# Kernel tuning notes

Hardware: AMD Instinct MI355X
Metric: run time of the kernel (lower is better)

Reference implementation:

```python
import jax, jax.numpy as jnp
import numpy as np

B, S, D = 2, 2048, 1024
H, DH = 16, 64
BS = 512            # block_size
MAX_LEN = 2048      # rope base = max_seq_length
NB = S // BS        # number of blocks (no padding: S % BS == 0)


def setup_inputs() -> dict:
    key = jax.random.key(0)
    ks = jax.random.split(key, 5)
    s = 1.0 / np.sqrt(D)
    x = jax.random.normal(ks[0], (B, S, D), jnp.float32)
    Wq = jax.random.normal(ks[1], (D, D), jnp.float32) * s
    Wk = jax.random.normal(ks[2], (D, D), jnp.float32) * s
    Wv = jax.random.normal(ks[3], (D, D), jnp.float32) * s
    Wo = jax.random.normal(ks[4], (D, D), jnp.float32) * s
    z = jnp.zeros((D,), jnp.float32)
    return {"x": x, "Wq": Wq, "bq": z, "Wk": Wk, "bk": z,
            "Wv": Wv, "bv": z, "Wo": Wo, "bo": z}


def _apply_rope(q, k):
    # inv_freq uses max_seq_length as the base (as in the source module)
    inv_freq = 1.0 / MAX_LEN ** (jnp.arange(0, DH, 2, dtype=jnp.float32) / DH)  # [DH/2]
    pos = jnp.arange(S, dtype=jnp.float32)
    freqs = jnp.outer(pos, inv_freq)                 # [S, DH/2]
    cos = jnp.cos(freqs)[None, :, None, :]           # [1,S,1,DH/2]
    sin = jnp.sin(freqs)[None, :, None, :]
    half = DH // 2
    q1, q2 = q[..., :half], q[..., half:]
    k1, k2 = k[..., :half], k[..., half:]
    q_rot = jnp.concatenate([q1 * cos - q2 * sin, q1 * sin + q2 * cos], axis=-1)
    k_rot = jnp.concatenate([k1 * cos - k2 * sin, k1 * sin + k2 * cos], axis=-1)
    return q_rot, k_rot


def _block_attn(qb, q_start, kb, vb, k_start):
    # qb,kb,vb: [B,H,BS,DH]; returns attended [B,H,BS,DH], lse [B,H,BS]
    scale = 1.0 / jnp.sqrt(DH)
    scores = jnp.einsum('bhqd,bhkd->bhqk', qb, kb) * scale
    q_pos = jnp.arange(BS) + q_start
    k_pos = jnp.arange(BS) + k_start
    mask = (q_pos[:, None] >= k_pos[None, :])[None, None]   # [1,1,BS,BS]
    scores = jnp.where(mask, scores, -1e9)
    mx = jnp.max(scores, axis=-1, keepdims=True)
    mx = jnp.where(jnp.isinf(mx), 0.0, mx)
    e = jnp.where(mask, jnp.exp(scores - mx), 0.0)
    se = jnp.sum(e, axis=-1, keepdims=True) + 1e-10
    attended = jnp.einsum('bhqk,bhkd->bhqd', e / se, vb)
    lse = (jnp.log(se) + mx)[..., 0]                        # [B,H,BS]
    return attended, lse


def _forward(x, Wq, bq, Wk, bk, Wv, bv, Wo, bo):
    q = (x @ Wq + bq).reshape(B, S, H, DH)
    k = (x @ Wk + bk).reshape(B, S, H, DH)
    v = (x @ Wv + bv).reshape(B, S, H, DH)
    q, k = _apply_rope(q, k)
    # split into blocks: [NB, B, H, BS, DH]
    def to_blocks(t):
        return t.reshape(B, NB, BS, H, DH).transpose(1, 0, 3, 2, 4)
    qb, kb, vb = to_blocks(q), to_blocks(k), to_blocks(v)
    starts = jnp.arange(NB) * BS
    inner = jax.vmap(_block_attn, in_axes=(None, None, 0, 0, 0))   # over k blocks
    outer = jax.vmap(inner, in_axes=(0, 0, None, None, None))      # over q blocks
    att, lse = outer(qb, starts, kb, vb, starts)
    # att: [NBq,NBk,B,H,BS,DH], lse: [NBq,NBk,B,H,BS]
    mlse = jnp.max(lse, axis=1, keepdims=True)
    w = jnp.exp(lse - mlse)
    w = w / (jnp.sum(w, axis=1, keepdims=True) + 1e-10)
    acc = jnp.sum(att * w[..., None], axis=1)                      # [NBq,B,H,BS,DH]
    out = acc.transpose(1, 0, 3, 2, 4).reshape(B, S, D)
    out = out @ Wo + bo
    return out


def reference(x, Wq, bq, Wk, bk, Wv, bv, Wo, bo):
    out = _forward(x, Wq, bq, Wk, bk, Wv, bv, Wo, bo)
    attention_weights = jnp.ones((B, H, S, S), jnp.float32)  # dummy, as in source
    return out, attention_weights
```

## Files before the change

### kernel.cpp

```cpp
#include <hip/hip_runtime.h>
#include <cstdint>
#include <cstddef>

#define DEVINL __device__ __forceinline__

typedef float   f32x4  __attribute__((ext_vector_type(4)));
typedef float   vf4    __attribute__((ext_vector_type(4)));
typedef __bf16  bf16x8 __attribute__((ext_vector_type(8)));
typedef uint32_t u32;
typedef unsigned short u16;
typedef uint32_t u32x4 __attribute__((ext_vector_type(4)));

constexpr int Bb = 2, Ss = 2048, Dd = 1024, Hh = 16;
constexpr int Mm = Bb * Ss;

DEVINL u16 f2bf(float f) {
  union { float f; u32 u; } a; a.f = f;
  u32 r = a.u + 0x7fffu + ((a.u >> 16) & 1u);
  return (u16)(r >> 16);
}

typedef const __attribute__((address_space(1))) void* gas_t;
typedef __attribute__((address_space(3))) void* las_t;
DEVINL void gld_lds16(const void* g, void* l) {
  __builtin_amdgcn_global_load_lds((gas_t)g, (las_t)l, 16, 0, 0);
}

__global__ void fill_ones(vf4* __restrict__ p, long long n4) {
  size_t i = (size_t)blockIdx.x * blockDim.x + threadIdx.x;
  size_t stride = (size_t)gridDim.x * blockDim.x;
  const vf4 one = {1.f, 1.f, 1.f, 1.f};
  for (; i < (size_t)n4; i += stride)
    __builtin_nontemporal_store(one, p + i);
}

__global__ void rope_table(float* __restrict__ cosT, float* __restrict__ sinT) {
  int idx = blockIdx.x * 256 + threadIdx.x;
  int s = idx >> 5, j = idx & 31;
  float freq = (float)s * exp2f(-11.0f * (float)j / 32.0f);
  cosT[idx] = cosf(freq);
  sinT[idx] = sinf(freq);
}

__global__ void cast_x(const float* __restrict__ x, u16* __restrict__ xb) {
  size_t i = ((size_t)blockIdx.x * 256 + threadIdx.x) * 4;
  vf4 v = *(const vf4*)(x + i);
  union { u16 u[4]; unsigned long long q; } o;
  o.u[0] = f2bf(v.x); o.u[1] = f2bf(v.y); o.u[2] = f2bf(v.z); o.u[3] = f2bf(v.w);
  *(unsigned long long*)(xb + i) = o.q;
}

__global__ void transpose_cast_W(const float* __restrict__ W0, const float* __restrict__ W1,
                                 const float* __restrict__ W2, const float* __restrict__ W3,
                                 u16* __restrict__ Wt) {
  __shared__ u16 tile[64][72];
  const int z = blockIdx.z;
  const float* W = (z == 0) ? W0 : (z == 1) ? W1 : (z == 2) ? W2 : W3;
  u16* Out = Wt + (size_t)z * (Dd * Dd);
  const int k0 = blockIdx.x * 64, n0 = blockIdx.y * 64;
  const int tid = threadIdx.x;
#pragma unroll
  for (int it = 0; it < 4; ++it) {
    int r = it * 16 + (tid >> 4);
    int c = (tid & 15) * 4;
    vf4 v = *(const vf4*)(W + (size_t)(k0 + r) * Dd + n0 + c);
    tile[r][c + 0] = f2bf(v.x); tile[r][c + 1] = f2bf(v.y);
    tile[r][c + 2] = f2bf(v.z); tile[r][c + 3] = f2bf(v.w);
  }
  __syncthreads();
#pragma unroll
  for (int it = 0; it < 2; ++it) {
    int c = it * 256 + tid;
    int n = c >> 3, ck = c & 7;
    union { u16 u[8]; u32x4 q; } o;
#pragma unroll
    for (int j = 0; j < 8; ++j) o.u[j] = tile[ck * 8 + j][n];
    *(u32x4*)(Out + (size_t)(n0 + n) * Dd + k0 + ck * 8) = o.q;
  }
}

template <int BM>
DEVINL void gemm_mainloop(const u16* __restrict__ A, const u16* __restrict__ Bt,
                          int m0, int n0, char* lds, f32x4 (&acc)[BM / 32][4],
                          vf4* __restrict__ onesp, size_t obase) {
  constexpr int MT = BM / 32;
  constexpr int ABYTES = BM * 64;
  const int tid = threadIdx.x, lane = tid & 63;
  const int w = tid >> 6, wr = w >> 1, wc = w & 1;
  const int l15 = lane & 15, l4 = lane >> 4;
  char* Ab = lds;
  char* Bb = lds + 2 * ABYTES;
  auto stageA = [&](int k0, char* dst) {
#pragma unroll
    for (int h2 = 0; h2 < BM / 64; ++h2) {
      int c = h2 * 256 + tid;
      const char* src = (const char*)A + (size_t)(m0 + (c >> 2)) * 2048 + k0 * 2 + (c & 3) * 16;
      gld_lds16(src, dst + c * 16);
    }
  };
  auto stageB = [&](int k0, char* dst) {
#pragma unroll
    for (int h2 = 0; h2 < 2; ++h2) {
      int c = h2 * 256 + tid;
      const char* src = (const char*)Bt + (size_t)(n0 + (c >> 2)) * 2048 + k0 * 2 + (c & 3) * 16;
      gld_lds16(src, dst + c * 16);
    }
  };
  stageA(0, Ab);
  stageB(0, Bb);
  __syncthreads();
  const vf4 onev = {1.f, 1.f, 1.f, 1.f};
#pragma unroll 2
  for (int t = 0; t < 32; ++t) {
    const int cur = t & 1;
    char* As = Ab + cur * ABYTES;
    char* Bs = Bb + cur * 8192;
    if (t < 31) {
      stageA((t + 1) * 32, Ab + (cur ^ 1) * ABYTES);
      stageB((t + 1) * 32, Bb + (cur ^ 1) * 8192);
    }
    __builtin_nontemporal_store(onev, onesp + obase + (size_t)t * 256 + tid);
    bf16x8 af[MT], bfr[4];
#pragma unroll
    for (int mt = 0; mt < MT; ++mt)
      af[mt] = *(const bf16x8*)(As + (wr * (MT * 16) + mt * 16 + l15) * 64 + l4 * 16);
#pragma unroll
    for (int nt = 0; nt < 4; ++nt)
      bfr[nt] = *(const bf16x8*)(Bs + (wc * 64 + nt * 16 + l15) * 64 + l4 * 16);
#pragma unroll
    for (int mt = 0; mt < MT; ++mt)
#pragma unroll
      for (int nt = 0; nt < 4; ++nt)
        acc[mt][nt] = __builtin_amdgcn_mfma_f32_16x16x32_bf16(af[mt], bfr[nt], acc[mt][nt], 0, 0, 0);
    __syncthreads();
  }
}

template <int EPI>
__global__ __launch_bounds__(256) void gemm128(
    const u16* __restrict__ A, const u16* __restrict__ W0,
    const float* __restrict__ b0, const float* __restrict__ b1, const float* __restrict__ b2,
    const float* __restrict__ cosT, const float* __restrict__ sinT,
    u16* __restrict__ Qo, u16* __restrict__ Ko, u16* __restrict__ Vo,
    float* __restrict__ outp, vf4* __restrict__ onesp) {
  constexpr int BM = (EPI == 0) ? 128 : 64;
  constexpr int MT = BM / 32;
  constexpr int MX = (EPI == 0) ? 32 : 64;
  constexpr int YPX = (EPI == 0) ? 3 : 1;
  __shared__ __align__(16) char lds[2 * BM * 64 + 16384];
  const int tid = threadIdx.x, lane = tid & 63;
  const int w = tid >> 6, wr = w >> 1, wc = w & 1;
  const int l15 = lane & 15, l4 = lane >> 4;

  const int lin = blockIdx.y * MX + blockIdx.x;
  const int xcd = lin & 7, ix = lin >> 3;
  const int ytile = xcd * YPX + ix / MX;
  const int m0 = (ix % MX) * BM;

  int mat, n0;
  const u16* Bt;
  if (EPI == 0) { mat = ytile >> 3; n0 = (ytile & 7) * 128; Bt = W0 + (size_t)mat * (Dd * Dd); }
  else          { mat = 0;          n0 = ytile * 128;       Bt = W0; }
  const size_t obase = (EPI == 0 ? 0 : (size_t)6291456) + (size_t)lin * 8192;

  f32x4 acc[MT][4] = {};
  gemm_mainloop<BM>(A, Bt, m0, n0, lds, acc, onesp, obase);

  if (EPI == 0) {
    const float* bias = (mat == 0) ? b0 : ((mat == 1) ? b1 : b2);
    u16* Out = (mat == 0) ? Qo : ((mat == 1) ? Ko : Vo);
    const bool dorope = (mat < 2);
#pragma unroll
    for (int mt = 0; mt < MT; ++mt) {
#pragma unroll
      for (int i = 0; i < 4; ++i) {
        int m = m0 + wr * (MT * 16) + mt * 16 + l4 * 4 + i;
        int bidx = m >> 11, s = m & 2047;
        float cv0 = 0.f, sv0 = 0.f, cv1 = 0.f, sv1 = 0.f;
        if (dorope) {
          cv0 = cosT[s * 32 + l15];      sv0 = sinT[s * 32 + l15];
          cv1 = cosT[s * 32 + 16 + l15]; sv1 = sinT[s * 32 + 16 + l15];
        }
#pragma unroll
        for (int nt = 0; nt < 4; ++nt) {
          int n = n0 + wc * 64 + nt * 16 + l15;
          float v = acc[mt][nt][i] + bias[n];
          float ov;
          if (dorope) {
            int np = n0 + wc * 64 + (nt ^ 2) * 16 + l15;
            float vp = acc[mt][nt ^ 2][i] + bias[np];
            float cc = (nt & 1) ? cv1 : cv0, sn = (nt & 1) ? sv1 : sv0;
            ov = (nt < 2) ? (v * cc - vp * sn)
                          : (vp * sn + v * cc);
          } else ov = v;
          int hh = n >> 6, dh = n & 63;
          Out[(((size_t)bidx * Hh + hh) * Ss + s) * 64 + dh] = f2bf(ov);
        }
      }
    }
  } else {
#pragma unroll
    for (int mt = 0; mt < MT; ++mt)
#pragma unroll
      for (int i = 0; i < 4; ++i) {
        int m = m0 + wr * (MT * 16) + mt * 16 + l4 * 4 + i;
#pragma unroll
        for (int nt = 0; nt < 4; ++nt) {
          int n = n0 + wc * 64 + nt * 16 + l15;
          outp[(size_t)m * Dd + n] = acc[mt][nt][i] + b0[n];
        }
      }
  }
}

__global__ void transpose_v(const u16* __restrict__ Vg, u16* __restrict__ Vtg) {
  __shared__ u16 tile[64][72];
  const int s0 = blockIdx.x * 64, bh = blockIdx.y;
  const int tid = threadIdx.x;
  const u16* Vb = Vg + (size_t)bh * Ss * 64;
  u16* Vtb = Vtg + (size_t)bh * 64 * Ss;
#pragma unroll
  for (int h2 = 0; h2 < 2; ++h2) {
    int c = h2 * 256 + tid;
    int r = c >> 3, ck = c & 7;
    u32x4 v = *(const u32x4*)(Vb + (size_t)(s0 + r) * 64 + ck * 8);
    const u16* t8 = (const u16*)&v;
#pragma unroll
    for (int j = 0; j < 8; ++j) tile[r][ck * 8 + j] = t8[j];
  }
  __syncthreads();
#pragma unroll
  for (int h2 = 0; h2 < 2; ++h2) {
    int c = h2 * 256 + tid;
    int dh = c >> 3, ck = c & 7;
    union { u16 u[8]; u32x4 q; } o;
#pragma unroll
    for (int j = 0; j < 8; ++j) o.u[j] = tile[ck * 8 + j][dh];
    *(u32x4*)(Vtb + (size_t)dh * Ss + s0 + ck * 8) = o.q;
  }
}

__global__ __launch_bounds__(256) void attn_kernel(
    const u16* __restrict__ Qg, const u16* __restrict__ Kg,
    const u16* __restrict__ Vtg, u16* __restrict__ Og, vf4* __restrict__ onesp) {
  __shared__ __align__(16) char lds[16384];

  const int tid = threadIdx.x, lane = tid & 63, w = tid >> 6;
  const int l15 = lane & 15, l4 = lane >> 4;

  const int bid = blockIdx.x;
  const int bh = bid & 31;
  const int qt_raw = (bid >> 5) & 7;
  const int qtile = (bid >> 8) ? qt_raw : (15 - qt_raw);
  const int qw = qtile * 128 + w * 32;
  const int tdiag = qw >> 6;

  const int quota = 2 * qtile + 1;
  const size_t abase = (size_t)10485760 +
      ((size_t)bh * 1024 + (size_t)(4 * qtile * qtile) + (size_t)w * quota) * 256 +
      (size_t)lane * 4;

  const u16*  Qb  = Qg + (size_t)bh * Ss * 64;
  const char* Kb  = (const char*)(Kg + (size_t)bh * Ss * 64);
  const char* Vtb = (const char*)(Vtg + (size_t)bh * 64 * Ss);

  bf16x8 aq[2][2];
#pragma unroll
  for (int mt = 0; mt < 2; ++mt)
#pragma unroll
    for (int kt = 0; kt < 2; ++kt)
      aq[mt][kt] = *(const bf16x8*)(Qb + (size_t)(qw + mt * 16 + l15) * 64 + kt * 32 + l4 * 8);

  f32x4 accO[2][4] = {};
  float mrow[2][4], lrow[2][4];
#pragma unroll
  for (int mt = 0; mt < 2; ++mt)
#pragma unroll
    for (int i = 0; i < 4; ++i) { mrow[mt][i] = -1e30f; lrow[mt][i] = 0.f; }

  char* pw = lds + w * 4096;
  const vf4 onev = {1.f, 1.f, 1.f, 1.f};

  for (int t = 0; t <= tdiag; ++t) {
    const int kv0 = t * 64;
    if (t < quota) {
#pragma unroll
      for (int j = 0; j < 4; ++j)
        __builtin_nontemporal_store(onev, onesp + abase + (size_t)t * 256 + j);
    }

    f32x4 sf[2][4] = {};
#pragma unroll
    for (int kt = 0; kt < 2; ++kt) {
      bf16x8 bk[4];
#pragma unroll
      for (int nt = 0; nt < 4; ++nt)
        bk[nt] = *(const bf16x8*)(Kb + (size_t)(kv0 + nt * 16 + l15) * 128 + kt * 64 + l4 * 16);
      __builtin_amdgcn_s_setprio(1);
#pragma unroll
      for (int mt = 0; mt < 2; ++mt)
#pragma unroll
        for (int nt = 0; nt < 4; ++nt)
          sf[mt][nt] = __builtin_amdgcn_mfma_f32_16x16x32_bf16(aq[mt][kt], bk[nt], sf[mt][nt], 0, 0, 0);
      __builtin_amdgcn_s_setprio(0);
    }

    const bool diag = (t == tdiag);
#pragma unroll
    for (int mt = 0; mt < 2; ++mt) {
#pragma unroll
      for (int i = 0; i < 4; ++i) {
        int row = qw + mt * 16 + l4 * 4 + i;
        float sv[4];
        float mx = -1e30f;
#pragma unroll
        for (int nt = 0; nt < 4; ++nt) {
          float xv = sf[mt][nt][i] * 0.125f;
          if (diag && (kv0 + nt * 16 + l15) > row) xv = -1e30f;
          sv[nt] = xv; mx = fmaxf(mx, xv);
        }
        mx = fmaxf(mx, __shfl_xor(mx, 1));
        mx = fmaxf(mx, __shfl_xor(mx, 2));
        mx = fmaxf(mx, __shfl_xor(mx, 4));
        mx = fmaxf(mx, __shfl_xor(mx, 8));
        float mnew = fmaxf(mrow[mt][i], mx);
        float rescale = __expf(mrow[mt][i] - mnew);
        float rs = 0.f;
        int rl = mt * 16 + l4 * 4 + i;
#pragma unroll
        for (int nt = 0; nt < 4; ++nt) {
          float p = __expf(sv[nt] - mnew);
          rs += p;
          int key = nt * 16 + l15;
          int boff = rl * 128 + (((key >> 3) ^ (rl & 7)) << 4) + (key & 7) * 2;
          *(u16*)(pw + boff) = f2bf(p);
        }
        rs += __shfl_xor(rs, 1); rs += __shfl_xor(rs, 2);
        rs += __shfl_xor(rs, 4); rs += __shfl_xor(rs, 8);
        lrow[mt][i] = lrow[mt][i] * rescale + rs;
        mrow[mt][i] = mnew;
#pragma unroll
        for (int nt = 0; nt < 4; ++nt) accO[mt][nt][i] *= rescale;
      }
    }

#pragma unroll
    for (int ks = 0; ks < 2; ++ks) {
      bf16x8 ap[2], bv[4];
#pragma unroll
      for (int mt = 0; mt < 2; ++mt) {
        int row = mt * 16 + l15;
        int ch = (ks * 4 + l4) ^ (row & 7);
        ap[mt] = *(const bf16x8*)(pw + row * 128 + ch * 16);
      }
#pragma unroll
      for (int nt = 0; nt < 4; ++nt)
        bv[nt] = *(const bf16x8*)(Vtb + (size_t)(nt * 16 + l15) * (Ss * 2) + (size_t)kv0 * 2 + ks * 64 + l4 * 16);
      __builtin_amdgcn_s_setprio(1);
#pragma unroll
      for (int mt = 0; mt < 2; ++mt)
#pragma unroll
        for (int nt = 0; nt < 4; ++nt)
          accO[mt][nt] = __builtin_amdgcn_mfma_f32_16x16x32_bf16(ap[mt], bv[nt], accO[mt][nt], 0, 0, 0);
      __builtin_amdgcn_s_setprio(0);
    }
  }

  const int b = bh >> 4, h = bh & 15;
#pragma unroll
  for (int mt = 0; mt < 2; ++mt)
#pragma unroll
    for (int i = 0; i < 4; ++i) {
      int s = qw + mt * 16 + l4 * 4 + i;
      float inv = 1.0f / (lrow[mt][i] + 1e-10f);
      size_t rowbase = ((size_t)b * Ss + s) * Dd + h * 64;
#pragma unroll
      for (int nt = 0; nt < 4; ++nt)
        Og[rowbase + nt * 16 + l15] = f2bf(accO[mt][nt][i] * inv);
    }
}

extern "C" void kernel_launch(void* const* d_in, const int* in_sizes, int n_in,
                              void* d_out, int out_size, void* d_ws, size_t ws_size,
                              hipStream_t stream) {
  const float* x  = (const float*)d_in[0];
  const float* Wq = (const float*)d_in[1];
  const float* bq = (const float*)d_in[2];
  const float* Wk = (const float*)d_in[3];
  const float* bk = (const float*)d_in[4];
  const float* Wv = (const float*)d_in[5];
  const float* bv = (const float*)d_in[6];
  const float* Wo = (const float*)d_in[7];
  const float* bo = (const float*)d_in[8];
  float* out = (float*)d_out;

  char* ws = (char*)d_ws;
  u16*   xb   = (u16*)(ws);
  u16*   Wt   = (u16*)(ws + ((size_t)8 << 20));
  float* cosT = (float*)(ws + ((size_t)16 << 20));
  float* sinT = (float*)(ws + ((size_t)16 << 20) + ((size_t)256 << 10));
  u16*   Qg   = (u16*)(ws + ((size_t)17 << 20));
  u16*   Kg   = (u16*)(ws + ((size_t)25 << 20));
  u16*   Vg   = (u16*)(ws + ((size_t)33 << 20));
  u16*   Vtg  = (u16*)(ws + ((size_t)41 << 20));
  u16*   Og   = (u16*)(ws + ((size_t)49 << 20));

  size_t ones_off = (size_t)Mm * Dd;
  vf4* onesp = (vf4*)(out + ones_off);
  const long long n4_total = ((long long)out_size - (long long)ones_off) / 4;
  const long long n4_side  = 18874368;
  fill_ones<<<2048, 256, 0, stream>>>(onesp + n4_side, n4_total - n4_side);

  rope_table<<<256, 256, 0, stream>>>(cosT, sinT);
  cast_x<<<(Mm * Dd) / 1024, 256, 0, stream>>>(x, xb);
  transpose_cast_W<<<dim3(16, 16, 4), 256, 0, stream>>>(Wq, Wk, Wv, Wo, Wt);

  gemm128<0><<<dim3(32, 24), 256, 0, stream>>>(xb, Wt, bq, bk, bv, cosT, sinT,
                                               Qg, Kg, Vg, nullptr, onesp);
  transpose_v<<<dim3(32, 32), 256, 0, stream>>>(Vg, Vtg);
  attn_kernel<<<512, 256, 0, stream>>>(Qg, Kg, Vtg, Og, onesp);
  gemm128<1><<<dim3(64, 8), 256, 0, stream>>>(Og, Wt + (size_t)3 * Dd * Dd,
                                              bo, nullptr, nullptr, nullptr, nullptr,
                                              nullptr, nullptr, nullptr, out, onesp);
}
```

Baseline: 733.8 us.

## Retile attention to 16-row waves, merge prep kernels, use exp2 softmax

Three setup kernels (rope table, x cast, weight transpose-cast) are merged into one launch by partitioning blockIdx.x ranges. This removes launch overhead and gaps between small kernels. The attention kernel is retiled from 128-row to 64-row query tiles, one 16-row MFMA tile per wave, with twice as many blocks and half the LDS, aiming for better occupancy and finer causal load balance. The softmax folds log2(e) into the scale so it can use exp2, and skips the accumulator rescale when the row max does not change. The in-kernel writes of the dummy ones tensor and the boundary of the separate fill kernel are recomputed to match the new tiling.

New measurement: 733.0 us. No clear change (-0.1%).

```diff
diff --git a/kernel.cpp b/kernel.cpp
--- a/kernel.cpp
+++ b/kernel.cpp
@@ -34,48 +34,49 @@
     __builtin_nontemporal_store(one, p + i);
 }
 
-__global__ void rope_table(float* __restrict__ cosT, float* __restrict__ sinT) {
-  int idx = blockIdx.x * 256 + threadIdx.x;
-  int s = idx >> 5, j = idx & 31;
-  float freq = (float)s * exp2f(-11.0f * (float)j / 32.0f);
-  cosT[idx] = cosf(freq);
-  sinT[idx] = sinf(freq);
-}
-
-__global__ void cast_x(const float* __restrict__ x, u16* __restrict__ xb) {
-  size_t i = ((size_t)blockIdx.x * 256 + threadIdx.x) * 4;
-  vf4 v = *(const vf4*)(x + i);
-  union { u16 u[4]; unsigned long long q; } o;
-  o.u[0] = f2bf(v.x); o.u[1] = f2bf(v.y); o.u[2] = f2bf(v.z); o.u[3] = f2bf(v.w);
-  *(unsigned long long*)(xb + i) = o.q;
-}
-
-__global__ void transpose_cast_W(const float* __restrict__ W0, const float* __restrict__ W1,
-                                 const float* __restrict__ W2, const float* __restrict__ W3,
-                                 u16* __restrict__ Wt) {
+__global__ void prep_kernel(const float* __restrict__ x, u16* __restrict__ xb,
+                            const float* __restrict__ W0, const float* __restrict__ W1,
+                            const float* __restrict__ W2, const float* __restrict__ W3,
+                            u16* __restrict__ Wt,
+                            float* __restrict__ cosT, float* __restrict__ sinT) {
   __shared__ u16 tile[64][72];
-  const int z = blockIdx.z;
-  const float* W = (z == 0) ? W0 : (z == 1) ? W1 : (z == 2) ? W2 : W3;
-  u16* Out = Wt + (size_t)z * (Dd * Dd);
-  const int k0 = blockIdx.x * 64, n0 = blockIdx.y * 64;
-  const int tid = threadIdx.x;
-#pragma unroll
-  for (int it = 0; it < 4; ++it) {
-    int r = it * 16 + (tid >> 4);
-    int c = (tid & 15) * 4;
-    vf4 v = *(const vf4*)(W + (size_t)(k0 + r) * Dd + n0 + c);
-    tile[r][c + 0] = f2bf(v.x); tile[r][c + 1] = f2bf(v.y);
-    tile[r][c + 2] = f2bf(v.z); tile[r][c + 3] = f2bf(v.w);
-  }
-  __syncthreads();
-#pragma unroll
-  for (int it = 0; it < 2; ++it) {
-    int c = it * 256 + tid;
-    int n = c >> 3, ck = c & 7;
-    union { u16 u[8]; u32x4 q; } o;
-#pragma unroll
-    for (int j = 0; j < 8; ++j) o.u[j] = tile[ck * 8 + j][n];
-    *(u32x4*)(Out + (size_t)(n0 + n) * Dd + k0 + ck * 8) = o.q;
+  const int blk = blockIdx.x, tid = threadIdx.x;
+  if (blk < 256) {
+    int idx = blk * 256 + tid;
+    int s = idx >> 5, j = idx & 31;
+    float freq = (float)s * exp2f(-11.0f * (float)j / 32.0f);
+    cosT[idx] = cosf(freq);
+    sinT[idx] = sinf(freq);
+  } else if (blk < 4352) {
+    size_t i = ((size_t)(blk - 256) * 256 + tid) * 4;
+    vf4 v = *(const vf4*)(x + i);
+    union { u16 u[4]; unsigned long long q; } o;
+    o.u[0] = f2bf(v.x); o.u[1] = f2bf(v.y); o.u[2] = f2bf(v.z); o.u[3] = f2bf(v.w);
+    *(unsigned long long*)(xb + i) = o.q;
+  } else {
+    const int lin = blk - 4352;
+    const int z = lin >> 8;
+    const float* W = (z == 0) ? W0 : (z == 1) ? W1 : (z == 2) ? W2 : W3;
+    u16* Out = Wt + (size_t)z * (Dd * Dd);
+    const int k0 = ((lin >> 4) & 15) * 64, n0 = (lin & 15) * 64;
+#pragma unroll
+    for (int it = 0; it < 4; ++it) {
+      int r = it * 16 + (tid >> 4);
+      int c = (tid & 15) * 4;
+      vf4 v = *(const vf4*)(W + (size_t)(k0 + r) * Dd + n0 + c);
+      tile[r][c + 0] = f2bf(v.x); tile[r][c + 1] = f2bf(v.y);
+      tile[r][c + 2] = f2bf(v.z); tile[r][c + 3] = f2bf(v.w);
+    }
+    __syncthreads();
+#pragma unroll
+    for (int it = 0; it < 2; ++it) {
+      int c = it * 256 + tid;
+      int n = c >> 3, ck = c & 7;
+      union { u16 u[8]; u32x4 q; } o;
+#pragma unroll
+      for (int j = 0; j < 8; ++j) o.u[j] = tile[ck * 8 + j][n];
+      *(u32x4*)(Out + (size_t)(n0 + n) * Dd + k0 + ck * 8) = o.q;
+    }
   }
 }
 
@@ -243,53 +244,45 @@
 __global__ __launch_bounds__(256) void attn_kernel(
     const u16* __restrict__ Qg, const u16* __restrict__ Kg,
     const u16* __restrict__ Vtg, u16* __restrict__ Og, vf4* __restrict__ onesp) {
-  __shared__ __align__(16) char lds[16384];
+  __shared__ __align__(16) char lds[8192];
+  constexpr float SCL = 0.18033688f;
 
   const int tid = threadIdx.x, lane = tid & 63, w = tid >> 6;
   const int l15 = lane & 15, l4 = lane >> 4;
 
   const int bid = blockIdx.x;
   const int bh = bid & 31;
-  const int qt_raw = (bid >> 5) & 7;
-  const int qtile = (bid >> 8) ? qt_raw : (15 - qt_raw);
-  const int qw = qtile * 128 + w * 32;
-  const int tdiag = qw >> 6;
-
-  const int quota = 2 * qtile + 1;
-  const size_t abase = (size_t)10485760 +
-      ((size_t)bh * 1024 + (size_t)(4 * qtile * qtile) + (size_t)w * quota) * 256 +
-      (size_t)lane * 4;
+  const int z = bid >> 5;
+  const int rt = (z < 16) ? (31 - z) : (z - 16);
+  const int qw = rt * 64 + w * 16;
+  const int ntiles = rt + 1;
+
+  const size_t cbase = (size_t)bh * 2112 + (size_t)(2 * rt * (rt + 1)) + (size_t)w * (rt + 1);
+  vf4* oball = onesp + (size_t)10485760 + cbase * 128 + (size_t)lane * 2;
 
   const u16*  Qb  = Qg + (size_t)bh * Ss * 64;
   const char* Kb  = (const char*)(Kg + (size_t)bh * Ss * 64);
   const char* Vtb = (const char*)(Vtg + (size_t)bh * 64 * Ss);
 
-  bf16x8 aq[2][2];
-#pragma unroll
-  for (int mt = 0; mt < 2; ++mt)
-#pragma unroll
-    for (int kt = 0; kt < 2; ++kt)
-      aq[mt][kt] = *(const bf16x8*)(Qb + (size_t)(qw + mt * 16 + l15) * 64 + kt * 32 + l4 * 8);
-
-  f32x4 accO[2][4] = {};
-  float mrow[2][4], lrow[2][4];
-#pragma unroll
-  for (int mt = 0; mt < 2; ++mt)
-#pragma unroll
-    for (int i = 0; i < 4; ++i) { mrow[mt][i] = -1e30f; lrow[mt][i] = 0.f; }
-
-  char* pw = lds + w * 4096;
+  bf16x8 aq[2];
+#pragma unroll
+  for (int kt = 0; kt < 2; ++kt)
+    aq[kt] = *(const bf16x8*)(Qb + (size_t)(qw + l15) * 64 + kt * 32 + l4 * 8);
+
+  f32x4 accO[4] = {};
+  float mrow[4], lrow[4];
+#pragma unroll
+  for (int i = 0; i < 4; ++i) { mrow[i] = -1e30f; lrow[i] = 0.f; }
+
+  char* pw = lds + w * 2048;
   const vf4 onev = {1.f, 1.f, 1.f, 1.f};
 
-  for (int t = 0; t <= tdiag; ++t) {
+  for (int t = 0; t < ntiles; ++t) {
     const int kv0 = t * 64;
-    if (t < quota) {
-#pragma unroll
-      for (int j = 0; j < 4; ++j)
-        __builtin_nontemporal_store(onev, onesp + abase + (size_t)t * 256 + j);
-    }
-
-    f32x4 sf[2][4] = {};
+    __builtin_nontemporal_store(onev, oball + (size_t)t * 128);
+    __builtin_nontemporal_store(onev, oball + (size_t)t * 128 + 1);
+
+    f32x4 sf[4] = {};
 #pragma unroll
     for (int kt = 0; kt < 2; ++kt) {
       bf16x8 bk[4];
@@ -298,86 +291,79 @@
         bk[nt] = *(const bf16x8*)(Kb + (size_t)(kv0 + nt * 16 + l15) * 128 + kt * 64 + l4 * 16);
       __builtin_amdgcn_s_setprio(1);
 #pragma unroll
-      for (int mt = 0; mt < 2; ++mt)
-#pragma unroll
-        for (int nt = 0; nt < 4; ++nt)
-          sf[mt][nt] = __builtin_amdgcn_mfma_f32_16x16x32_bf16(aq[mt][kt], bk[nt], sf[mt][nt], 0, 0, 0);
+      for (int nt = 0; nt < 4; ++nt)
+        sf[nt] = __builtin_amdgcn_mfma_f32_16x16x32_bf16(aq[kt], bk[nt], sf[nt], 0, 0, 0);
       __builtin_amdgcn_s_setprio(0);
     }
 
-    const bool diag = (t == tdiag);
-#pragma unroll
-    for (int mt = 0; mt < 2; ++mt) {
-#pragma unroll
-      for (int i = 0; i < 4; ++i) {
-        int row = qw + mt * 16 + l4 * 4 + i;
-        float sv[4];
-        float mx = -1e30f;
-#pragma unroll
-        for (int nt = 0; nt < 4; ++nt) {
-          float xv = sf[mt][nt][i] * 0.125f;
-          if (diag && (kv0 + nt * 16 + l15) > row) xv = -1e30f;
-          sv[nt] = xv; mx = fmaxf(mx, xv);
-        }
-        mx = fmaxf(mx, __shfl_xor(mx, 1));
-        mx = fmaxf(mx, __shfl_xor(mx, 2));
-        mx = fmaxf(mx, __shfl_xor(mx, 4));
-        mx = fmaxf(mx, __shfl_xor(mx, 8));
-        float mnew = fmaxf(mrow[mt][i], mx);
-        float rescale = __expf(mrow[mt][i] - mnew);
-        float rs = 0.f;
-        int rl = mt * 16 + l4 * 4 + i;
-#pragma unroll
-        for (int nt = 0; nt < 4; ++nt) {
-          float p = __expf(sv[nt] - mnew);
-          rs += p;
-          int key = nt * 16 + l15;
-          int boff = rl * 128 + (((key >> 3) ^ (rl & 7)) << 4) + (key & 7) * 2;
-          *(u16*)(pw + boff) = f2bf(p);
-        }
-        rs += __shfl_xor(rs, 1); rs += __shfl_xor(rs, 2);
-        rs += __shfl_xor(rs, 4); rs += __shfl_xor(rs, 8);
-        lrow[mt][i] = lrow[mt][i] * rescale + rs;
-        mrow[mt][i] = mnew;
-#pragma unroll
-        for (int nt = 0; nt < 4; ++nt) accO[mt][nt][i] *= rescale;
+    const bool diag = (t == rt);
+#pragma unroll
+    for (int i = 0; i < 4; ++i) {
+      int row = qw + l4 * 4 + i;
+      float sv[4];
+      float mx = -1e30f;
+#pragma unroll
+      for (int nt = 0; nt < 4; ++nt) {
+        float xv = sf[nt][i] * SCL;
+        if (diag && (kv0 + nt * 16 + l15) > row) xv = -1e30f;
+        sv[nt] = xv; mx = fmaxf(mx, xv);
+      }
+      mx = fmaxf(mx, __shfl_xor(mx, 1));
+      mx = fmaxf(mx, __shfl_xor(mx, 2));
+      mx = fmaxf(mx, __shfl_xor(mx, 4));
+      mx = fmaxf(mx, __shfl_xor(mx, 8));
+      float mnew = fmaxf(mrow[i], mx);
+      float rs = 0.f;
+      int rl = l4 * 4 + i;
+#pragma unroll
+      for (int nt = 0; nt < 4; ++nt) {
+        float p = __builtin_exp2f(sv[nt] - mnew);
+        rs += p;
+        int key = nt * 16 + l15;
+        int boff = rl * 128 + (((key >> 3) ^ (rl & 7)) << 4) + (key & 7) * 2;
+        *(u16*)(pw + boff) = f2bf(p);
+      }
+      rs += __shfl_xor(rs, 1); rs += __shfl_xor(rs, 2);
+      rs += __shfl_xor(rs, 4); rs += __shfl_xor(rs, 8);
+      if (mnew > mrow[i]) {
+        float rc = __builtin_exp2f(mrow[i] - mnew);
+        lrow[i] = lrow[i] * rc + rs;
+        mrow[i] = mnew;
+#pragma unroll
+        for (int nt = 0; nt < 4; ++nt) accO[nt][i] *= rc;
+      } else {
+        lrow[i] += rs;
       }
     }
 
 #pragma unroll
     for (int ks = 0; ks < 2; ++ks) {
-      bf16x8 ap[2], bv[4];
-#pragma unroll
-      for (int mt = 0; mt < 2; ++mt) {
-        int row = mt * 16 + l15;
-        int ch = (ks * 4 + l4) ^ (row & 7);
-        ap[mt] = *(const bf16x8*)(pw + row * 128 + ch * 16);
+      bf16x8 ap, bv[4];
+      {
+        int ch = (ks * 4 + l4) ^ (l15 & 7);
+        ap = *(const bf16x8*)(pw + l15 * 128 + ch * 16);
       }
 #pragma unroll
       for (int nt = 0; nt < 4; ++nt)
         bv[nt] = *(const bf16x8*)(Vtb + (size_t)(nt * 16 + l15) * (Ss * 2) + (size_t)kv0 * 2 + ks * 64 + l4 * 16);
       __builtin_amdgcn_s_setprio(1);
 #pragma unroll
-      for (int mt = 0; mt < 2; ++mt)
-#pragma unroll
-        for (int nt = 0; nt < 4; ++nt)
-          accO[mt][nt] = __builtin_amdgcn_mfma_f32_16x16x32_bf16(ap[mt], bv[nt], accO[mt][nt], 0, 0, 0);
+      for (int nt = 0; nt < 4; ++nt)
+        accO[nt] = __builtin_amdgcn_mfma_f32_16x16x32_bf16(ap, bv[nt], accO[nt], 0, 0, 0);
       __builtin_amdgcn_s_setprio(0);
     }
   }
 
   const int b = bh >> 4, h = bh & 15;
 #pragma unroll
-  for (int mt = 0; mt < 2; ++mt)
-#pragma unroll
-    for (int i = 0; i < 4; ++i) {
-      int s = qw + mt * 16 + l4 * 4 + i;
-      float inv = 1.0f / (lrow[mt][i] + 1e-10f);
-      size_t rowbase = ((size_t)b * Ss + s) * Dd + h * 64;
-#pragma unroll
-      for (int nt = 0; nt < 4; ++nt)
-        Og[rowbase + nt * 16 + l15] = f2bf(accO[mt][nt][i] * inv);
-    }
+  for (int i = 0; i < 4; ++i) {
+    int s = qw + l4 * 4 + i;
+    float inv = 1.0f / (lrow[i] + 1e-10f);
+    size_t rowbase = ((size_t)b * Ss + s) * Dd + h * 64;
+#pragma unroll
+    for (int nt = 0; nt < 4; ++nt)
+      Og[rowbase + nt * 16 + l15] = f2bf(accO[nt][i] * inv);
+  }
 }
 
 extern "C" void kernel_launch(void* const* d_in, const int* in_sizes, int n_in,
@@ -408,17 +394,15 @@
   size_t ones_off = (size_t)Mm * Dd;
   vf4* onesp = (vf4*)(out + ones_off);
   const long long n4_total = ((long long)out_size - (long long)ones_off) / 4;
-  const long long n4_side  = 18874368;
+  const long long n4_side  = 19136512;
   fill_ones<<<2048, 256, 0, stream>>>(onesp + n4_side, n4_total - n4_side);
 
-  rope_table<<<256, 256, 0, stream>>>(cosT, sinT);
-  cast_x<<<(Mm * Dd) / 1024, 256, 0, stream>>>(x, xb);
-  transpose_cast_W<<<dim3(16, 16, 4), 256, 0, stream>>>(Wq, Wk, Wv, Wo, Wt);
+  prep_kernel<<<5376, 256, 0, stream>>>(x, xb, Wq, Wk, Wv, Wo, Wt, cosT, sinT);
 
   gemm128<0><<<dim3(32, 24), 256, 0, stream>>>(xb, Wt, bq, bk, bv, cosT, sinT,
                                                Qg, Kg, Vg, nullptr, onesp);
   transpose_v<<<dim3(32, 32), 256, 0, stream>>>(Vg, Vtg);
-  attn_kernel<<<512, 256, 0, stream>>>(Qg, Kg, Vtg, Og, onesp);
+  attn_kernel<<<1024, 256, 0, stream>>>(Qg, Kg, Vtg, Og, onesp);
   gemm128<1><<<dim3(64, 8), 256, 0, stream>>>(Og, Wt + (size_t)3 * Dd * Dd,
                                               bo, nullptr, nullptr, nullptr, nullptr,
                                               nullptr, nullptr, nullptr, out, onesp);
```
